# Kernel optimization log

Hardware: AMD Instinct MI355X
Metric: run time of the kernel (lower is better)

## Reference

```python
import jax, jax.numpy as jnp
import numpy as np

N_NODES = 100000
N_EDGES = 1600000
D_IN = 64
D_OUT = 64
NUM_ETYPE = 2
NEG_SLOPE = 0.2


def setup_inputs() -> dict:
    key = jax.random.key(0)
    ks = jax.random.split(key, 9)
    feat = jax.random.normal(ks[0], (N_NODES, D_IN), dtype=jnp.float32)
    rel = jax.random.uniform(ks[1], (N_EDGES, NUM_ETYPE), dtype=jnp.float32)
    W_self = jax.random.normal(ks[2], (D_OUT, D_IN), dtype=jnp.float32) * 0.1
    b_self = jax.random.normal(ks[3], (D_OUT,), dtype=jnp.float32) * 0.1
    W_neigh = jax.random.normal(ks[4], (D_OUT, D_IN), dtype=jnp.float32) * 0.1
    b_neigh = jax.random.normal(ks[5], (D_OUT,), dtype=jnp.float32) * 0.1
    attn_e = jax.random.normal(ks[6], (NUM_ETYPE, 1), dtype=jnp.float32)
    src = jax.random.randint(ks[7], (N_EDGES,), 0, N_NODES, dtype=jnp.int32)
    dst = jax.random.randint(ks[8], (N_EDGES,), 0, N_NODES, dtype=jnp.int32)
    return {"feat": feat, "rel": rel, "W_self": W_self, "b_self": b_self,
            "W_neigh": W_neigh, "b_neigh": b_neigh, "attn_e": attn_e,
            "src": src, "dst": dst}


def reference(feat, rel, W_self, b_self, W_neigh, b_neigh, attn_e, src, dst):
    n = feat.shape[0]
    # per-edge attention score: [E, num_etype] @ [num_etype, 1] -> [E]
    e = jnp.squeeze(rel @ attn_e, axis=1)
    e = jax.nn.leaky_relu(e, negative_slope=NEG_SLOPE)
    # edge_softmax: segment softmax over edges grouped by destination node
    emax = jax.ops.segment_max(e, dst, num_segments=n)          # [N]
    ex = jnp.exp(e - emax[dst])                                  # [E]
    denom = jax.ops.segment_sum(ex, dst, num_segments=n)        # [N]
    a = ex / denom[dst]                                          # [E]
    # u_mul_e + sum aggregation: neigh[v] = sum_e a_e * feat[src_e]
    m = feat[src] * a[:, None]                                   # [E, D_IN]
    h_neigh = jax.ops.segment_sum(m, dst, num_segments=n)       # [N, D_IN]
    # rst = fc_self(h_self) + fc_neigh(h_neigh)  (torch Linear: x @ W.T + b)
    return feat @ W_self.T + b_self + h_neigh @ W_neigh.T + b_neigh
```

## Files before the change

kernel.cpp:

```cpp
#include <hip/hip_runtime.h>
#include <hip/hip_bf16.h>
#include <hip/hip_fp16.h>

#define N_NODES 100000
#define N_EDGES 1600000
#define D 64
#define NEG_SLOPE 0.2f

#define BSHIFT 9
#define BNODES 512
#define NBUCK ((N_NODES + BNODES - 1) >> BSHIFT)
#define BUCKET_CAP 8896
#define P1_EPB 4096
#define P1_T 512
#define P1_IT (P1_EPB / P1_T)
#define GRID_BIN ((N_EDGES + P1_EPB - 1) / P1_EPB)
#define GEMM_BLKS ((N_NODES + 127) / 128)

typedef __attribute__((ext_vector_type(8))) short bf16x8;
typedef __attribute__((ext_vector_type(4))) float f32x4;
#define MFMA16(a, b, c) __builtin_amdgcn_mfma_f32_16x16x32_bf16(a, b, c, 0, 0, 0)

__device__ __forceinline__ short bf16_rne(float f) {
    unsigned u = __float_as_uint(f);
    u += 0x7FFFu + ((u >> 16) & 1u);
    return (short)(u >> 16);
}
__device__ __forceinline__ float bf16_to_f(short h) {
    return __uint_as_float(((unsigned)(unsigned short)h) << 16);
}
__device__ __forceinline__ void cvt8(float4 f0, float4 f1,
                                     bf16x8& hi, bf16x8& lo) {
    float v[8] = {f0.x, f0.y, f0.z, f0.w, f1.x, f1.y, f1.z, f1.w};
    #pragma unroll
    for (int j = 0; j < 8; ++j) {
        short h = bf16_rne(v[j]);
        hi[j] = h;
        lo[j] = bf16_rne(v[j] - bf16_to_f(h));
    }
}

#define SM_BYTES 35152

__global__ __launch_bounds__(P1_T) void fused_bin_gemm_kernel(
    const float2* __restrict__ rel, const float* __restrict__ attn_e,
    const int* __restrict__ src, const int* __restrict__ dst,
    int* __restrict__ bucket_cursor, uint2* __restrict__ binned,
    const float* __restrict__ feat,
    const float* __restrict__ W_self, const float* __restrict__ W_neigh,
    const float* __restrict__ b_self, const float* __restrict__ b_neigh,
    float* __restrict__ out, __half* __restrict__ g)
{
    __shared__ __align__(16) char smem[SM_BYTES];
    int tid = threadIdx.x;

    if (blockIdx.x >= GRID_BIN) {
        bf16x8* wfrag = (bf16x8*)smem;
        float* bsum = (float*)(smem + 32768);
        if (tid < D) bsum[tid] = b_self[tid] + b_neigh[tid];
        for (int c = tid; c < 1024; c += P1_T) {
            int nt = c >> 8;
            int mat = (c >> 7) & 1;
            int s = (c >> 6) & 1;
            int ln = c & 63;
            const float* Wm = mat ? W_neigh : W_self;
            int row = nt * 16 + (ln & 15);
            int koff = s * 32 + (ln >> 4) * 8;
            const float4* p = (const float4*)(Wm + row * D + koff);
            bf16x8 hi, lo;
            cvt8(p[0], p[1], hi, lo);
            int base = (c >> 6) * 128 + ln;
            wfrag[base] = hi;
            wfrag[base + 64] = lo;
        }
        __syncthreads();

        int lane = tid & 63;
        int wave = tid >> 6;
        int llo = lane & 15;
        int lhi = lane >> 4;
        int rb = (blockIdx.x - GRID_BIN) * 128 + wave * 16;
        if (rb >= N_NODES) return;

        int node = rb + llo;
        bool valid = node < N_NODES;
        int nclamp = valid ? node : N_NODES - 1;
        const float4* fr = (const float4*)(feat + (size_t)nclamp * D);
        bf16x8 fhi[2], flo[2];
        #pragma unroll
        for (int s = 0; s < 2; ++s)
            cvt8(fr[s * 8 + lhi * 2], fr[s * 8 + lhi * 2 + 1], fhi[s], flo[s]);

        const float4* bs4 = (const float4*)bsum;
        #pragma unroll
        for (int nt = 0; nt < 4; ++nt) {
            int base = nt * 512 + lane;
            bf16x8 wSh0 = wfrag[base];
            bf16x8 wSl0 = wfrag[base + 64];
            bf16x8 wSh1 = wfrag[base + 128];
            bf16x8 wSl1 = wfrag[base + 192];
            bf16x8 wNh0 = wfrag[base + 256];
            bf16x8 wNl0 = wfrag[base + 320];
            bf16x8 wNh1 = wfrag[base + 384];
            bf16x8 wNl1 = wfrag[base + 448];
            f32x4 accS = {0.f, 0.f, 0.f, 0.f};
            f32x4 accN = {0.f, 0.f, 0.f, 0.f};
            accS = MFMA16(wSh0, fhi[0], accS);
            accN = MFMA16(wNh0, fhi[0], accN);
            accS = MFMA16(wSl0, fhi[0], accS);
            accN = MFMA16(wNl0, fhi[0], accN);
            accS = MFMA16(wSh0, flo[0], accS);
            accN = MFMA16(wNh0, flo[0], accN);
            accS = MFMA16(wSh1, fhi[1], accS);
            accN = MFMA16(wNh1, fhi[1], accN);
            accS = MFMA16(wSl1, fhi[1], accS);
            accN = MFMA16(wNl1, fhi[1], accN);
            accS = MFMA16(wSh1, flo[1], accS);
            accN = MFMA16(wNh1, flo[1], accN);

            if (valid) {
                float4 bb = bs4[nt * 4 + lhi];
                float4 o;
                o.x = accS[0] + bb.x;
                o.y = accS[1] + bb.y;
                o.z = accS[2] + bb.z;
                o.w = accS[3] + bb.w;
                *(float4*)(out + (size_t)node * D + nt * 16 + lhi * 4) = o;
                __half2 hA = __floats2half2_rn(accN[0], accN[1]);
                __half2 hB = __floats2half2_rn(accN[2], accN[3]);
                uint2 gp = make_uint2(*(unsigned*)&hA, *(unsigned*)&hB);
                *(uint2*)(g + (size_t)node * D + nt * 16 + lhi * 4) = gp;
            }
        }
        return;
    }

    uint2* staged2 = (uint2*)smem;
    int* cnt = (int*)(smem + 32768);
    int* excl = (int*)(smem + 32768 + 784);
    int* chunkbase = (int*)(smem + 32768 + 1568);
    int* wtot = (int*)(smem + 32768 + 2352);

    int e0 = blockIdx.x * P1_EPB;
    int n = min(P1_EPB, N_EDGES - e0);

    for (int b = tid; b < NBUCK; b += P1_T) cnt[b] = 0;
    __syncthreads();

    float a0 = attn_e[0], a1 = attn_e[1];

    uint2 ev[P1_IT];
    int myslot[P1_IT];
    #pragma unroll
    for (int j = 0; j < P1_IT; ++j) {
        int i = tid + j * P1_T;
        if (i < n) {
            int e = e0 + i;
            float2 r = rel[e];
            float sc = r.x * a0 + r.y * a1;
            sc = (sc > 0.f) ? sc : NEG_SLOPE * sc;
            float evx = __expf(sc);
            unsigned u = __float_as_uint(evx) + 0x8000u;
            unsigned wcode = (u >> 16) & 0x7FFFu;
            unsigned s = (unsigned)src[e];
            unsigned d = (unsigned)dst[e];
            ev[j] = make_uint2((s << 15) | wcode, d);
            myslot[j] = atomicAdd(&cnt[d >> BSHIFT], 1);
        }
    }
    __syncthreads();
    {
        int ln = tid & 63, wv = tid >> 6;
        int c = 0;
        if (tid < 256) c = (tid < NBUCK) ? cnt[tid] : 0;
        int x = c;
        #pragma unroll
        for (int dd = 1; dd < 64; dd <<= 1) {
            int y = __shfl_up(x, dd, 64);
            if (ln >= dd) x += y;
        }
        if (tid < 256 && ln == 63) wtot[wv] = x;
        __syncthreads();
        if (tid < NBUCK) {
            int wbase = 0;
            for (int k = 0; k < wv; ++k) wbase += wtot[k];
            excl[tid] = wbase + x - c;
        }
        __syncthreads();
    }
    #pragma unroll
    for (int j = 0; j < P1_IT; ++j) {
        int i = tid + j * P1_T;
        if (i < n)
            staged2[excl[ev[j].y >> BSHIFT] + myslot[j]] = ev[j];
    }
    if (tid < NBUCK)
        chunkbase[tid] = atomicAdd(&bucket_cursor[tid], cnt[tid]);
    __syncthreads();
    for (int i = tid; i < n; i += P1_T) {
        uint2 v = staged2[i];
        int b = (int)(v.y >> BSHIFT);
        binned[(size_t)b * BUCKET_CAP + chunkbase[b] + (i - excl[b])] = v;
    }
}

__global__ __launch_bounds__(1024) void csr_kernel(
    const int* __restrict__ bucket_cursor, const uint2* __restrict__ binned,
    int* __restrict__ offsets, unsigned* __restrict__ edata)
{
    __shared__ unsigned vals[BUCKET_CAP];
    __shared__ int hist[BNODES];
    __shared__ int nexcl[BNODES];
    __shared__ int cur[BNODES];
    __shared__ int bc[NBUCK];
    __shared__ int wtot[8];
    __shared__ int base_sh;

    int b = blockIdx.x;
    int tid = threadIdx.x;

    if (tid < NBUCK) bc[tid] = bucket_cursor[tid];
    if (tid < BNODES) { hist[tid] = 0; cur[tid] = 0; }
    __syncthreads();
    if (tid == 0) {
        int s = 0;
        for (int i = 0; i < b; ++i) s += bc[i];
        base_sh = s;
    }
    __syncthreads();
    int count = bc[b];
    int base = base_sh;
    const uint2* bin = binned + (size_t)b * BUCKET_CAP;

    for (int i = tid; i < count; i += 1024)
        atomicAdd(&hist[bin[i].y & (BNODES - 1)], 1);
    __syncthreads();

    {
        int ln = tid & 63, wv = tid >> 6;
        int h = 0;
        if (tid < BNODES) h = hist[tid];
        int x = h;
        #pragma unroll
        for (int dd = 1; dd < 64; dd <<= 1) {
            int y = __shfl_up(x, dd, 64);
            if (ln >= dd) x += y;
        }
        if (tid < BNODES && ln == 63) wtot[wv] = x;
        __syncthreads();
        if (tid < BNODES) {
            int wbase = 0;
            for (int k = 0; k < wv; ++k) wbase += wtot[k];
            nexcl[tid] = wbase + x - h;
        }
        __syncthreads();
    }

    int node = (b << BSHIFT) + tid;
    if (tid < BNODES && node < N_NODES) offsets[node] = base + nexcl[tid];
    if (b == NBUCK - 1 && tid == 0) offsets[N_NODES] = N_EDGES;

    for (int i = tid; i < count; i += 1024) {
        uint2 e = bin[i];
        int d = e.y & (BNODES - 1);
        int t = atomicAdd(&cur[d], 1);
        vals[nexcl[d] + t] = e.x;
    }
    __syncthreads();
    for (int i = tid; i < count; i += 1024)
        edata[base + i] = vals[i];
}

__global__ __launch_bounds__(256) void aggregate_kernel(
    const __half* __restrict__ g, const unsigned* __restrict__ edata,
    const int* __restrict__ offsets, float* __restrict__ out)
{
    int v = blockIdx.x * 4 + (threadIdx.x >> 6);
    int lane = threadIdx.x & 63;
    int q = lane >> 3;
    int t = lane & 7;
    int lo = offsets[v], hi = offsets[v + 1];
    float4 acc0 = make_float4(0.f, 0.f, 0.f, 0.f);
    float4 acc1 = make_float4(0.f, 0.f, 0.f, 0.f);
    float sum = 0.f;

    for (int i = lo; i < hi; i += 16) {
        int e0 = i + q;
        int e1 = i + 8 + q;
        int ec0 = (e0 < hi) ? e0 : hi - 1;
        int ec1 = (e1 < hi) ? e1 : hi - 1;
        unsigned p0 = edata[ec0];
        unsigned p1 = edata[ec1];
        float w0 = (e0 < hi) ? __uint_as_float((p0 & 0x7FFFu) << 16) : 0.f;
        float w1 = (e1 < hi) ? __uint_as_float((p1 & 0x7FFFu) << 16) : 0.f;
        const uint4* r0 = (const uint4*)(g + (size_t)(p0 >> 15) * D);
        const uint4* r1 = (const uint4*)(g + (size_t)(p1 >> 15) * D);
        uint4 u0 = r0[t];
        uint4 u1 = r1[t];
        {
            float2 f;
            f = __half22float2(*(const __half2*)&u0.x);
            acc0.x = fmaf(w0, f.x, acc0.x); acc0.y = fmaf(w0, f.y, acc0.y);
            f = __half22float2(*(const __half2*)&u0.y);
            acc0.z = fmaf(w0, f.x, acc0.z); acc0.w = fmaf(w0, f.y, acc0.w);
            f = __half22float2(*(const __half2*)&u0.z);
            acc1.x = fmaf(w0, f.x, acc1.x); acc1.y = fmaf(w0, f.y, acc1.y);
            f = __half22float2(*(const __half2*)&u0.w);
            acc1.z = fmaf(w0, f.x, acc1.z); acc1.w = fmaf(w0, f.y, acc1.w);
            sum += w0;
        }
        {
            float2 f;
            f = __half22float2(*(const __half2*)&u1.x);
            acc0.x = fmaf(w1, f.x, acc0.x); acc0.y = fmaf(w1, f.y, acc0.y);
            f = __half22float2(*(const __half2*)&u1.y);
            acc0.z = fmaf(w1, f.x, acc0.z); acc0.w = fmaf(w1, f.y, acc0.w);
            f = __half22float2(*(const __half2*)&u1.z);
            acc1.x = fmaf(w1, f.x, acc1.x); acc1.y = fmaf(w1, f.y, acc1.y);
            f = __half22float2(*(const __half2*)&u1.w);
            acc1.z = fmaf(w1, f.x, acc1.z); acc1.w = fmaf(w1, f.y, acc1.w);
            sum += w1;
        }
    }
    #pragma unroll
    for (int mm = 8; mm <= 32; mm <<= 1) {
        acc0.x += __shfl_xor(acc0.x, mm, 64);
        acc0.y += __shfl_xor(acc0.y, mm, 64);
        acc0.z += __shfl_xor(acc0.z, mm, 64);
        acc0.w += __shfl_xor(acc0.w, mm, 64);
        acc1.x += __shfl_xor(acc1.x, mm, 64);
        acc1.y += __shfl_xor(acc1.y, mm, 64);
        acc1.z += __shfl_xor(acc1.z, mm, 64);
        acc1.w += __shfl_xor(acc1.w, mm, 64);
        sum   += __shfl_xor(sum,   mm, 64);
    }
    if (hi > lo && q == 0) {
        float inv = 1.f / sum;
        float4* orow = (float4*)(out + (size_t)v * D);
        float4 c0 = orow[2 * t];
        float4 c1 = orow[2 * t + 1];
        c0.x += acc0.x * inv; c0.y += acc0.y * inv;
        c0.z += acc0.z * inv; c0.w += acc0.w * inv;
        c1.x += acc1.x * inv; c1.y += acc1.y * inv;
        c1.z += acc1.z * inv; c1.w += acc1.w * inv;
        orow[2 * t] = c0;
        orow[2 * t + 1] = c1;
    }
}

extern "C" void kernel_launch(void* const* d_in, const int* in_sizes, int n_in,
                              void* d_out, int out_size, void* d_ws, size_t ws_size,
                              hipStream_t stream) {
    const float* feat    = (const float*)d_in[0];
    const float* rel     = (const float*)d_in[1];
    const float* W_self  = (const float*)d_in[2];
    const float* b_self  = (const float*)d_in[3];
    const float* W_neigh = (const float*)d_in[4];
    const float* b_neigh = (const float*)d_in[5];
    const float* attn_e  = (const float*)d_in[6];
    const int*   src     = (const int*)d_in[7];
    const int*   dst     = (const int*)d_in[8];
    float* out = (float*)d_out;

    uint2* binned = (uint2*)d_ws;
    __half* g = (__half*)(binned + (size_t)NBUCK * BUCKET_CAP);
    unsigned* edata = (unsigned*)((char*)g + (size_t)N_NODES * D * 2);
    int* offsets = (int*)(edata + N_EDGES);
    int* bucket_cursor = offsets + N_NODES + 1;

    hipMemsetAsync(bucket_cursor, 0, NBUCK * sizeof(int), stream);

    fused_bin_gemm_kernel<<<GRID_BIN + GEMM_BLKS, P1_T, 0, stream>>>(
        (const float2*)rel, attn_e, src, dst, bucket_cursor, binned,
        feat, W_self, W_neigh, b_self, b_neigh, out, g);
    csr_kernel<<<NBUCK, 1024, 0, stream>>>(
        bucket_cursor, binned, offsets, edata);
    aggregate_kernel<<<N_NODES / 4, 256, 0, stream>>>(
        g, edata, offsets, out);
}
```

Measured before the change: 177.5 us.

## Move dense GEMM blocks from binning kernel into CSR kernel launch

Splits the binning phase into its own kernel and moves the node-wise MFMA GEMM blocks into the CSR-building launch, using 1024-thread blocks that each cover 256 nodes. The CSR kernel's shared arrays are carved out of one shared buffer so both block roles fit a single kernel. The goal is to overlap the GEMM with the light, low-occupancy CSR stage (196 blocks) rather than with the heavier binning stage. The GEMM blocks now run at 1024 threads with larger shared memory, which may change occupancy and scheduling balance.

```diff
diff --git a/kernel.cpp b/kernel.cpp
--- a/kernel.cpp
+++ b/kernel.cpp
@@ -15,7 +15,7 @@
 #define P1_T 512
 #define P1_IT (P1_EPB / P1_T)
 #define GRID_BIN ((N_EDGES + P1_EPB - 1) / P1_EPB)
-#define GEMM_BLKS ((N_NODES + 127) / 128)
+#define GEMM2_BLKS ((N_NODES + 255) / 256)
 
 typedef __attribute__((ext_vector_type(8))) short bf16x8;
 typedef __attribute__((ext_vector_type(4))) float f32x4;
@@ -40,25 +40,101 @@
     }
 }
 
-#define SM_BYTES 35152
-
-__global__ __launch_bounds__(P1_T) void fused_bin_gemm_kernel(
+#define SM_BIN 35152
+__global__ __launch_bounds__(P1_T) void binning_kernel(
     const float2* __restrict__ rel, const float* __restrict__ attn_e,
     const int* __restrict__ src, const int* __restrict__ dst,
-    int* __restrict__ bucket_cursor, uint2* __restrict__ binned,
+    int* __restrict__ bucket_cursor, uint2* __restrict__ binned)
+{
+    __shared__ __align__(16) char smem[SM_BIN];
+    uint2* staged2 = (uint2*)smem;
+    int* cnt = (int*)(smem + 32768);
+    int* excl = (int*)(smem + 32768 + 784);
+    int* chunkbase = (int*)(smem + 32768 + 1568);
+    int* wtot = (int*)(smem + 32768 + 2352);
+    int tid = threadIdx.x;
+
+    int e0 = blockIdx.x * P1_EPB;
+    int n = min(P1_EPB, N_EDGES - e0);
+
+    for (int b = tid; b < NBUCK; b += P1_T) cnt[b] = 0;
+    __syncthreads();
+
+    float a0 = attn_e[0], a1 = attn_e[1];
+
+    uint2 ev[P1_IT];
+    int myslot[P1_IT];
+    #pragma unroll
+    for (int j = 0; j < P1_IT; ++j) {
+        int i = tid + j * P1_T;
+        if (i < n) {
+            int e = e0 + i;
+            float2 r = rel[e];
+            float sc = r.x * a0 + r.y * a1;
+            sc = (sc > 0.f) ? sc : NEG_SLOPE * sc;
+            float evx = __expf(sc);
+            unsigned u = __float_as_uint(evx) + 0x8000u;
+            unsigned wcode = (u >> 16) & 0x7FFFu;
+            unsigned s = (unsigned)src[e];
+            unsigned d = (unsigned)dst[e];
+            ev[j] = make_uint2((s << 15) | wcode, d);
+            myslot[j] = atomicAdd(&cnt[d >> BSHIFT], 1);
+        }
+    }
+    __syncthreads();
+    {
+        int ln = tid & 63, wv = tid >> 6;
+        int c = 0;
+        if (tid < 256) c = (tid < NBUCK) ? cnt[tid] : 0;
+        int x = c;
+        #pragma unroll
+        for (int dd = 1; dd < 64; dd <<= 1) {
+            int y = __shfl_up(x, dd, 64);
+            if (ln >= dd) x += y;
+        }
+        if (tid < 256 && ln == 63) wtot[wv] = x;
+        __syncthreads();
+        if (tid < NBUCK) {
+            int wbase = 0;
+            for (int k = 0; k < wv; ++k) wbase += wtot[k];
+            excl[tid] = wbase + x - c;
+        }
+        __syncthreads();
+    }
+    #pragma unroll
+    for (int j = 0; j < P1_IT; ++j) {
+        int i = tid + j * P1_T;
+        if (i < n)
+            staged2[excl[ev[j].y >> BSHIFT] + myslot[j]] = ev[j];
+    }
+    if (tid < NBUCK)
+        chunkbase[tid] = atomicAdd(&bucket_cursor[tid], cnt[tid]);
+    __syncthreads();
+    for (int i = tid; i < n; i += P1_T) {
+        uint2 v = staged2[i];
+        int b = (int)(v.y >> BSHIFT);
+        binned[(size_t)b * BUCKET_CAP + chunkbase[b] + (i - excl[b])] = v;
+    }
+}
+
+#define SM2_BYTES 42560
+
+__global__ __launch_bounds__(1024) void csr_gemm_kernel(
+    const int* __restrict__ bucket_cursor, const uint2* __restrict__ binned,
+    int* __restrict__ offsets, unsigned* __restrict__ edata,
     const float* __restrict__ feat,
     const float* __restrict__ W_self, const float* __restrict__ W_neigh,
     const float* __restrict__ b_self, const float* __restrict__ b_neigh,
     float* __restrict__ out, __half* __restrict__ g)
 {
-    __shared__ __align__(16) char smem[SM_BYTES];
+    __shared__ __align__(16) char smem[SM2_BYTES];
     int tid = threadIdx.x;
 
-    if (blockIdx.x >= GRID_BIN) {
+    if (blockIdx.x >= NBUCK) {
         bf16x8* wfrag = (bf16x8*)smem;
         float* bsum = (float*)(smem + 32768);
         if (tid < D) bsum[tid] = b_self[tid] + b_neigh[tid];
-        for (int c = tid; c < 1024; c += P1_T) {
+        for (int c = tid; c < 1024; c += 1024) {
             int nt = c >> 8;
             int mat = (c >> 7) & 1;
             int s = (c >> 6) & 1;
@@ -79,7 +155,7 @@
         int wave = tid >> 6;
         int llo = lane & 15;
         int lhi = lane >> 4;
-        int rb = (blockIdx.x - GRID_BIN) * 128 + wave * 16;
+        int rb = (blockIdx.x - NBUCK) * 256 + wave * 16;
         if (rb >= N_NODES) return;
 
         int node = rb + llo;
@@ -135,89 +211,15 @@
         return;
     }
 
-    uint2* staged2 = (uint2*)smem;
-    int* cnt = (int*)(smem + 32768);
-    int* excl = (int*)(smem + 32768 + 784);
-    int* chunkbase = (int*)(smem + 32768 + 1568);
-    int* wtot = (int*)(smem + 32768 + 2352);
-
-    int e0 = blockIdx.x * P1_EPB;
-    int n = min(P1_EPB, N_EDGES - e0);
-
-    for (int b = tid; b < NBUCK; b += P1_T) cnt[b] = 0;
-    __syncthreads();
-
-    float a0 = attn_e[0], a1 = attn_e[1];
-
-    uint2 ev[P1_IT];
-    int myslot[P1_IT];
-    #pragma unroll
-    for (int j = 0; j < P1_IT; ++j) {
-        int i = tid + j * P1_T;
-        if (i < n) {
-            int e = e0 + i;
-            float2 r = rel[e];
-            float sc = r.x * a0 + r.y * a1;
-            sc = (sc > 0.f) ? sc : NEG_SLOPE * sc;
-            float evx = __expf(sc);
-            unsigned u = __float_as_uint(evx) + 0x8000u;
-            unsigned wcode = (u >> 16) & 0x7FFFu;
-            unsigned s = (unsigned)src[e];
-            unsigned d = (unsigned)dst[e];
-            ev[j] = make_uint2((s << 15) | wcode, d);
-            myslot[j] = atomicAdd(&cnt[d >> BSHIFT], 1);
-        }
-    }
-    __syncthreads();
-    {
-        int ln = tid & 63, wv = tid >> 6;
-        int c = 0;
-        if (tid < 256) c = (tid < NBUCK) ? cnt[tid] : 0;
-        int x = c;
-        #pragma unroll
-        for (int dd = 1; dd < 64; dd <<= 1) {
-            int y = __shfl_up(x, dd, 64);
-            if (ln >= dd) x += y;
-        }
-        if (tid < 256 && ln == 63) wtot[wv] = x;
-        __syncthreads();
-        if (tid < NBUCK) {
-            int wbase = 0;
-            for (int k = 0; k < wv; ++k) wbase += wtot[k];
-            excl[tid] = wbase + x - c;
-        }
-        __syncthreads();
-    }
-    #pragma unroll
-    for (int j = 0; j < P1_IT; ++j) {
-        int i = tid + j * P1_T;
-        if (i < n)
-            staged2[excl[ev[j].y >> BSHIFT] + myslot[j]] = ev[j];
-    }
-    if (tid < NBUCK)
-        chunkbase[tid] = atomicAdd(&bucket_cursor[tid], cnt[tid]);
-    __syncthreads();
-    for (int i = tid; i < n; i += P1_T) {
-        uint2 v = staged2[i];
-        int b = (int)(v.y >> BSHIFT);
-        binned[(size_t)b * BUCKET_CAP + chunkbase[b] + (i - excl[b])] = v;
-    }
-}
-
-__global__ __launch_bounds__(1024) void csr_kernel(
-    const int* __restrict__ bucket_cursor, const uint2* __restrict__ binned,
-    int* __restrict__ offsets, unsigned* __restrict__ edata)
-{
-    __shared__ unsigned vals[BUCKET_CAP];
-    __shared__ int hist[BNODES];
-    __shared__ int nexcl[BNODES];
-    __shared__ int cur[BNODES];
-    __shared__ int bc[NBUCK];
-    __shared__ int wtot[8];
-    __shared__ int base_sh;
+    unsigned* vals = (unsigned*)smem;
+    int* hist = (int*)(smem + 35584);
+    int* nexcl = (int*)(smem + 37632);
+    int* cur = (int*)(smem + 39680);
+    int* bc = (int*)(smem + 41728);
+    int* wtot = (int*)(smem + 42512);
+    int* base_sh = (int*)(smem + 42544);
 
     int b = blockIdx.x;
-    int tid = threadIdx.x;
 
     if (tid < NBUCK) bc[tid] = bucket_cursor[tid];
     if (tid < BNODES) { hist[tid] = 0; cur[tid] = 0; }
@@ -225,11 +227,11 @@
     if (tid == 0) {
         int s = 0;
         for (int i = 0; i < b; ++i) s += bc[i];
-        base_sh = s;
+        *base_sh = s;
     }
     __syncthreads();
     int count = bc[b];
-    int base = base_sh;
+    int base = *base_sh;
     const uint2* bin = binned + (size_t)b * BUCKET_CAP;
 
     for (int i = tid; i < count; i += 1024)
@@ -370,11 +372,11 @@
 
     hipMemsetAsync(bucket_cursor, 0, NBUCK * sizeof(int), stream);
 
-    fused_bin_gemm_kernel<<<GRID_BIN + GEMM_BLKS, P1_T, 0, stream>>>(
-        (const float2*)rel, attn_e, src, dst, bucket_cursor, binned,
+    binning_kernel<<<GRID_BIN, P1_T, 0, stream>>>(
+        (const float2*)rel, attn_e, src, dst, bucket_cursor, binned);
+    csr_gemm_kernel<<<NBUCK + GEMM2_BLKS, 1024, 0, stream>>>(
+        bucket_cursor, binned, offsets, edata,
         feat, W_self, W_neigh, b_self, b_neigh, out, g);
-    csr_kernel<<<NBUCK, 1024, 0, stream>>>(
-        bucket_cursor, binned, offsets, edata);
     aggregate_kernel<<<N_NODES / 4, 256, 0, stream>>>(
         g, edata, offsets, out);
 }
```

New measurement: 183.4 us. +3.3%, slower.

## Split CSR buckets across two blocks and aggregate two nodes per wavefront

Applied to the files above, without the earlier changes.

The CSR build now launches two blocks per 512-node bucket. Each block handles one 256-node half, filtering edges by a destination bit, which doubles the number of CSR blocks and halves their shared-memory footprint. The aggregation kernel now processes two adjacent destination nodes per wavefront, interleaving their gathers to raise memory-level parallelism. In exchange, each CSR block reads the whole bucket twice, and in aggregation the node with fewer edges runs masked loads until the longer one finishes.

```diff
diff --git a/kernel.cpp b/kernel.cpp
--- a/kernel.cpp
+++ b/kernel.cpp
@@ -16,6 +16,9 @@
 #define P1_IT (P1_EPB / P1_T)
 #define GRID_BIN ((N_EDGES + P1_EPB - 1) / P1_EPB)
 #define GEMM_BLKS ((N_NODES + 127) / 128)
+
+#define HNODES 256
+#define HCAP 4672
 
 typedef __attribute__((ext_vector_type(8))) short bf16x8;
 typedef __attribute__((ext_vector_type(4))) float f32x4;
@@ -208,19 +211,20 @@
     const int* __restrict__ bucket_cursor, const uint2* __restrict__ binned,
     int* __restrict__ offsets, unsigned* __restrict__ edata)
 {
-    __shared__ unsigned vals[BUCKET_CAP];
-    __shared__ int hist[BNODES];
-    __shared__ int nexcl[BNODES];
-    __shared__ int cur[BNODES];
+    __shared__ unsigned vals[HCAP];
+    __shared__ int hist[HNODES];
+    __shared__ int nexcl[HNODES];
+    __shared__ int cur[HNODES];
     __shared__ int bc[NBUCK];
-    __shared__ int wtot[8];
-    __shared__ int base_sh;
-
-    int b = blockIdx.x;
+    __shared__ int wtot[4];
+    __shared__ int base_sh, htot_sh;
+
     int tid = threadIdx.x;
+    int b = blockIdx.x >> 1;
+    unsigned half = blockIdx.x & 1;
 
     if (tid < NBUCK) bc[tid] = bucket_cursor[tid];
-    if (tid < BNODES) { hist[tid] = 0; cur[tid] = 0; }
+    if (tid < HNODES) { hist[tid] = 0; cur[tid] = 0; }
     __syncthreads();
     if (tid == 0) {
         int s = 0;
@@ -229,45 +233,54 @@
     }
     __syncthreads();
     int count = bc[b];
-    int base = base_sh;
     const uint2* bin = binned + (size_t)b * BUCKET_CAP;
 
-    for (int i = tid; i < count; i += 1024)
-        atomicAdd(&hist[bin[i].y & (BNODES - 1)], 1);
+    for (int i = tid; i < count; i += 1024) {
+        unsigned d = bin[i].y;
+        if (((d >> 8) & 1u) == half)
+            atomicAdd(&hist[d & (HNODES - 1)], 1);
+    }
     __syncthreads();
 
     {
         int ln = tid & 63, wv = tid >> 6;
-        int h = 0;
-        if (tid < BNODES) h = hist[tid];
-        int x = h;
-        #pragma unroll
-        for (int dd = 1; dd < 64; dd <<= 1) {
-            int y = __shfl_up(x, dd, 64);
-            if (ln >= dd) x += y;
-        }
-        if (tid < BNODES && ln == 63) wtot[wv] = x;
+        int h = 0, x = 0;
+        if (tid < HNODES) {
+            h = hist[tid];
+            x = h;
+            #pragma unroll
+            for (int dd = 1; dd < 64; dd <<= 1) {
+                int y = __shfl_up(x, dd, 64);
+                if (ln >= dd) x += y;
+            }
+            if (ln == 63) wtot[wv] = x;
+        }
         __syncthreads();
-        if (tid < BNODES) {
+        if (tid < HNODES) {
             int wbase = 0;
             for (int k = 0; k < wv; ++k) wbase += wtot[k];
             nexcl[tid] = wbase + x - h;
+            if (tid == HNODES - 1) htot_sh = wbase + x;
         }
         __syncthreads();
     }
-
-    int node = (b << BSHIFT) + tid;
-    if (tid < BNODES && node < N_NODES) offsets[node] = base + nexcl[tid];
-    if (b == NBUCK - 1 && tid == 0) offsets[N_NODES] = N_EDGES;
+    int hcount = htot_sh;
+    int base = base_sh + (half ? (count - hcount) : 0);
+
+    int node = (b << BSHIFT) + (int)half * HNODES + tid;
+    if (tid < HNODES && node < N_NODES) offsets[node] = base + nexcl[tid];
+    if (b == NBUCK - 1 && half == 1 && tid == 0) offsets[N_NODES] = N_EDGES;
 
     for (int i = tid; i < count; i += 1024) {
         uint2 e = bin[i];
-        int d = e.y & (BNODES - 1);
-        int t = atomicAdd(&cur[d], 1);
-        vals[nexcl[d] + t] = e.x;
-    }
-    __syncthreads();
-    for (int i = tid; i < count; i += 1024)
+        if (((e.y >> 8) & 1u) == half) {
+            int d = e.y & (HNODES - 1);
+            int t = atomicAdd(&cur[d], 1);
+            vals[nexcl[d] + t] = e.x;
+        }
+    }
+    __syncthreads();
+    for (int i = tid; i < hcount; i += 1024)
         edata[base + i] = vals[i];
 }
 
@@ -275,74 +288,122 @@
     const __half* __restrict__ g, const unsigned* __restrict__ edata,
     const int* __restrict__ offsets, float* __restrict__ out)
 {
-    int v = blockIdx.x * 4 + (threadIdx.x >> 6);
+    int w = blockIdx.x * 4 + (threadIdx.x >> 6);
+    int vA = w * 2, vB = vA + 1;
     int lane = threadIdx.x & 63;
     int q = lane >> 3;
     int t = lane & 7;
-    int lo = offsets[v], hi = offsets[v + 1];
-    float4 acc0 = make_float4(0.f, 0.f, 0.f, 0.f);
-    float4 acc1 = make_float4(0.f, 0.f, 0.f, 0.f);
-    float sum = 0.f;
-
-    for (int i = lo; i < hi; i += 16) {
-        int e0 = i + q;
-        int e1 = i + 8 + q;
-        int ec0 = (e0 < hi) ? e0 : hi - 1;
-        int ec1 = (e1 < hi) ? e1 : hi - 1;
-        unsigned p0 = edata[ec0];
-        unsigned p1 = edata[ec1];
-        float w0 = (e0 < hi) ? __uint_as_float((p0 & 0x7FFFu) << 16) : 0.f;
-        float w1 = (e1 < hi) ? __uint_as_float((p1 & 0x7FFFu) << 16) : 0.f;
-        const uint4* r0 = (const uint4*)(g + (size_t)(p0 >> 15) * D);
-        const uint4* r1 = (const uint4*)(g + (size_t)(p1 >> 15) * D);
-        uint4 u0 = r0[t];
-        uint4 u1 = r1[t];
-        {
-            float2 f;
-            f = __half22float2(*(const __half2*)&u0.x);
-            acc0.x = fmaf(w0, f.x, acc0.x); acc0.y = fmaf(w0, f.y, acc0.y);
-            f = __half22float2(*(const __half2*)&u0.y);
-            acc0.z = fmaf(w0, f.x, acc0.z); acc0.w = fmaf(w0, f.y, acc0.w);
-            f = __half22float2(*(const __half2*)&u0.z);
-            acc1.x = fmaf(w0, f.x, acc1.x); acc1.y = fmaf(w0, f.y, acc1.y);
-            f = __half22float2(*(const __half2*)&u0.w);
-            acc1.z = fmaf(w0, f.x, acc1.z); acc1.w = fmaf(w0, f.y, acc1.w);
-            sum += w0;
-        }
-        {
-            float2 f;
-            f = __half22float2(*(const __half2*)&u1.x);
-            acc0.x = fmaf(w1, f.x, acc0.x); acc0.y = fmaf(w1, f.y, acc0.y);
-            f = __half22float2(*(const __half2*)&u1.y);
-            acc0.z = fmaf(w1, f.x, acc0.z); acc0.w = fmaf(w1, f.y, acc0.w);
-            f = __half22float2(*(const __half2*)&u1.z);
-            acc1.x = fmaf(w1, f.x, acc1.x); acc1.y = fmaf(w1, f.y, acc1.y);
-            f = __half22float2(*(const __half2*)&u1.w);
-            acc1.z = fmaf(w1, f.x, acc1.z); acc1.w = fmaf(w1, f.y, acc1.w);
-            sum += w1;
-        }
+    int loA = offsets[vA];
+    int mid = offsets[vB];
+    int hiB = offsets[vB + 1];
+    int hiA = mid, loB = mid;
+
+    float4 a0 = make_float4(0.f,0.f,0.f,0.f), a1 = make_float4(0.f,0.f,0.f,0.f);
+    float4 b0 = make_float4(0.f,0.f,0.f,0.f), b1 = make_float4(0.f,0.f,0.f,0.f);
+    float sumA = 0.f, sumB = 0.f;
+
+    int iA = loA, iB = loB;
+    while (iA < hiA || iB < hiB) {
+        int eA0 = iA + q,     eA1 = iA + 8 + q;
+        int eB0 = iB + q,     eB1 = iB + 8 + q;
+        int cA0 = min(eA0, N_EDGES - 1);
+        int cA1 = min(eA1, N_EDGES - 1);
+        int cB0 = min(eB0, N_EDGES - 1);
+        int cB1 = min(eB1, N_EDGES - 1);
+        unsigned pA0 = edata[cA0];
+        unsigned pA1 = edata[cA1];
+        unsigned pB0 = edata[cB0];
+        unsigned pB1 = edata[cB1];
+        float wA0 = (eA0 < hiA) ? __uint_as_float((pA0 & 0x7FFFu) << 16) : 0.f;
+        float wA1 = (eA1 < hiA) ? __uint_as_float((pA1 & 0x7FFFu) << 16) : 0.f;
+        float wB0 = (eB0 < hiB) ? __uint_as_float((pB0 & 0x7FFFu) << 16) : 0.f;
+        float wB1 = (eB1 < hiB) ? __uint_as_float((pB1 & 0x7FFFu) << 16) : 0.f;
+        uint4 uA0 = ((const uint4*)(g + (size_t)(pA0 >> 15) * D))[t];
+        uint4 uA1 = ((const uint4*)(g + (size_t)(pA1 >> 15) * D))[t];
+        uint4 uB0 = ((const uint4*)(g + (size_t)(pB0 >> 15) * D))[t];
+        uint4 uB1 = ((const uint4*)(g + (size_t)(pB1 >> 15) * D))[t];
+        float2 f;
+        f = __half22float2(*(const __half2*)&uA0.x);
+        a0.x = fmaf(wA0, f.x, a0.x); a0.y = fmaf(wA0, f.y, a0.y);
+        f = __half22float2(*(const __half2*)&uA0.y);
+        a0.z = fmaf(wA0, f.x, a0.z); a0.w = fmaf(wA0, f.y, a0.w);
+        f = __half22float2(*(const __half2*)&uA0.z);
+        a1.x = fmaf(wA0, f.x, a1.x); a1.y = fmaf(wA0, f.y, a1.y);
+        f = __half22float2(*(const __half2*)&uA0.w);
+        a1.z = fmaf(wA0, f.x, a1.z); a1.w = fmaf(wA0, f.y, a1.w);
+        sumA += wA0;
+        f = __half22float2(*(const __half2*)&uA1.x);
+        a0.x = fmaf(wA1, f.x, a0.x); a0.y = fmaf(wA1, f.y, a0.y);
+        f = __half22float2(*(const __half2*)&uA1.y);
+        a0.z = fmaf(wA1, f.x, a0.z); a0.w = fmaf(wA1, f.y, a0.w);
+        f = __half22float2(*(const __half2*)&uA1.z);
+        a1.x = fmaf(wA1, f.x, a1.x); a1.y = fmaf(wA1, f.y, a1.y);
+        f = __half22float2(*(const __half2*)&uA1.w);
+        a1.z = fmaf(wA1, f.x, a1.z); a1.w = fmaf(wA1, f.y, a1.w);
+        sumA += wA1;
+        f = __half22float2(*(const __half2*)&uB0.x);
+        b0.x = fmaf(wB0, f.x, b0.x); b0.y = fmaf(wB0, f.y, b0.y);
+        f = __half22float2(*(const __half2*)&uB0.y);
+        b0.z = fmaf(wB0, f.x, b0.z); b0.w = fmaf(wB0, f.y, b0.w);
+        f = __half22float2(*(const __half2*)&uB0.z);
+        b1.x = fmaf(wB0, f.x, b1.x); b1.y = fmaf(wB0, f.y, b1.y);
+        f = __half22float2(*(const __half2*)&uB0.w);
+        b1.z = fmaf(wB0, f.x, b1.z); b1.w = fmaf(wB0, f.y, b1.w);
+        sumB += wB0;
+        f = __half22float2(*(const __half2*)&uB1.x);
+        b0.x = fmaf(wB1, f.x, b0.x); b0.y = fmaf(wB1, f.y, b0.y);
+        f = __half22float2(*(const __half2*)&uB1.y);
+        b0.z = fmaf(wB1, f.x, b0.z); b0.w = fmaf(wB1, f.y, b0.w);
+        f = __half22float2(*(const __half2*)&uB1.z);
+        b1.x = fmaf(wB1, f.x, b1.x); b1.y = fmaf(wB1, f.y, b1.y);
+        f = __half22float2(*(const __half2*)&uB1.w);
+        b1.z = fmaf(wB1, f.x, b1.z); b1.w = fmaf(wB1, f.y, b1.w);
+        sumB += wB1;
+        iA += 16;
+        iB += 16;
     }
     #pragma unroll
     for (int mm = 8; mm <= 32; mm <<= 1) {
-        acc0.x += __shfl_xor(acc0.x, mm, 64);
-        acc0.y += __shfl_xor(acc0.y, mm, 64);
-        acc0.z += __shfl_xor(acc0.z, mm, 64);
-        acc0.w += __shfl_xor(acc0.w, mm, 64);
-        acc1.x += __shfl_xor(acc1.x, mm, 64);
-        acc1.y += __shfl_xor(acc1.y, mm, 64);
-        acc1.z += __shfl_xor(acc1.z, mm, 64);
-        acc1.w += __shfl_xor(acc1.w, mm, 64);
-        sum   += __shfl_xor(sum,   mm, 64);
-    }
-    if (hi > lo && q == 0) {
-        float inv = 1.f / sum;
-        float4* orow = (float4*)(out + (size_t)v * D);
+        a0.x += __shfl_xor(a0.x, mm, 64);
+        a0.y += __shfl_xor(a0.y, mm, 64);
+        a0.z += __shfl_xor(a0.z, mm, 64);
+        a0.w += __shfl_xor(a0.w, mm, 64);
+        a1.x += __shfl_xor(a1.x, mm, 64);
+        a1.y += __shfl_xor(a1.y, mm, 64);
+        a1.z += __shfl_xor(a1.z, mm, 64);
+        a1.w += __shfl_xor(a1.w, mm, 64);
+        sumA  += __shfl_xor(sumA,  mm, 64);
+        b0.x += __shfl_xor(b0.x, mm, 64);
+        b0.y += __shfl_xor(b0.y, mm, 64);
+        b0.z += __shfl_xor(b0.z, mm, 64);
+        b0.w += __shfl_xor(b0.w, mm, 64);
+        b1.x += __shfl_xor(b1.x, mm, 64);
+        b1.y += __shfl_xor(b1.y, mm, 64);
+        b1.z += __shfl_xor(b1.z, mm, 64);
+        b1.w += __shfl_xor(b1.w, mm, 64);
+        sumB  += __shfl_xor(sumB,  mm, 64);
+    }
+    if (hiA > loA && q == 0) {
+        float inv = 1.f / sumA;
+        float4* orow = (float4*)(out + (size_t)vA * D);
         float4 c0 = orow[2 * t];
         float4 c1 = orow[2 * t + 1];
-        c0.x += acc0.x * inv; c0.y += acc0.y * inv;
-        c0.z += acc0.z * inv; c0.w += acc0.w * inv;
-        c1.x += acc1.x * inv; c1.y += acc1.y * inv;
-        c1.z += acc1.z * inv; c1.w += acc1.w * inv;
+        c0.x += a0.x * inv; c0.y += a0.y * inv;
+        c0.z += a0.z * inv; c0.w += a0.w * inv;
+        c1.x += a1.x * inv; c1.y += a1.y * inv;
+        c1.z += a1.z * inv; c1.w += a1.w * inv;
+        orow[2 * t] = c0;
+        orow[2 * t + 1] = c1;
+    }
+    if (hiB > loB && q == 0) {
+        float inv = 1.f / sumB;
+        float4* orow = (float4*)(out + (size_t)vB * D);
+        float4 c0 = orow[2 * t];
+        float4 c1 = orow[2 * t + 1];
+        c0.x += b0.x * inv; c0.y += b0.y * inv;
+        c0.z += b0.z * inv; c0.w += b0.w * inv;
+        c1.x += b1.x * inv; c1.y += b1.y * inv;
+        c1.z += b1.z * inv; c1.w += b1.w * inv;
         orow[2 * t] = c0;
         orow[2 * t + 1] = c1;
     }
@@ -373,8 +434,8 @@
     fused_bin_gemm_kernel<<<GRID_BIN + GEMM_BLKS, P1_T, 0, stream>>>(
         (const float2*)rel, attn_e, src, dst, bucket_cursor, binned,
         feat, W_self, W_neigh, b_self, b_neigh, out, g);
-    csr_kernel<<<NBUCK, 1024, 0, stream>>>(
+    csr_kernel<<<NBUCK * 2, 1024, 0, stream>>>(
         bucket_cursor, binned, offsets, edata);
-    aggregate_kernel<<<N_NODES / 4, 256, 0, stream>>>(
+    aggregate_kernel<<<N_NODES / 8, 256, 0, stream>>>(
         g, edata, offsets, out);
 }
```

Result: no change. 179.5 us (+1.2%).
